# Performance work log

Hardware: AMD Instinct MI355X
Metric: run time of the kernel (lower is better)

## Reference

```python
import jax, jax.numpy as jnp
import numpy as np

DIM_INPUT = 1024
DIM_LATENT = 1024
DIM_HEAD = 64
INNER = max(DIM_INPUT, DIM_LATENT)  # 1024
HEADS = INNER // DIM_HEAD           # 16
SCALE = DIM_HEAD ** -0.5
RMS_EPS = 1e-8
LN_EPS = 1e-5


def layernorm(x, w, b):
    mu = jnp.mean(x, axis=-1, keepdims=True)
    var = jnp.var(x, axis=-1, keepdims=True)
    return (x - mu) * jax.lax.rsqrt(var + LN_EPS) * w + b


def rmsnorm(x, gamma):
    # x / clamp(||x||_2 * d^-0.5, eps) * gamma  (per-head, last dim = DIM_HEAD)
    norm = jnp.linalg.norm(x, axis=-1, keepdims=True) * (DIM_HEAD ** -0.5)
    return x / jnp.maximum(norm, RMS_EPS) * gamma


def setup_inputs() -> dict:
    key = jax.random.key(0)
    ks = jax.random.split(key, 10)
    b, n, m = 4, 2048, 256
    x = jax.random.normal(ks[0], (b, n, DIM_INPUT), dtype=jnp.float32)
    latents_c1 = jax.random.normal(ks[1], (b, m, DIM_LATENT), dtype=jnp.float32)
    latents_c0 = jax.random.normal(ks[2], (b, m, DIM_LATENT), dtype=jnp.float32)
    consciousness_mask = jax.random.randint(ks[3], (b, n), 0, 2).astype(bool)
    s = 0.02
    Wq = jax.random.normal(ks[4], (DIM_LATENT, INNER), dtype=jnp.float32) * s
    Wkv = jax.random.normal(ks[5], (DIM_INPUT, 2 * INNER), dtype=jnp.float32) * s
    Wout = jax.random.normal(ks[6], (INNER, DIM_LATENT), dtype=jnp.float32) * s
    bout = jnp.zeros((DIM_LATENT,), dtype=jnp.float32)
    ln_x_w = jnp.ones((DIM_INPUT,), dtype=jnp.float32)
    ln_x_b = jnp.zeros((DIM_INPUT,), dtype=jnp.float32)
    ln_l_w = jnp.ones((DIM_LATENT,), dtype=jnp.float32)
    ln_l_b = jnp.zeros((DIM_LATENT,), dtype=jnp.float32)
    gamma_q = jnp.ones((DIM_HEAD,), dtype=jnp.float32)
    gamma_k = jnp.ones((DIM_HEAD,), dtype=jnp.float32)
    return dict(x=x, latents_c1=latents_c1, latents_c0=latents_c0,
                consciousness_mask=consciousness_mask,
                ln_x_w=ln_x_w, ln_x_b=ln_x_b, ln_l_w=ln_l_w, ln_l_b=ln_l_b,
                gamma_q=gamma_q, gamma_k=gamma_k,
                Wq=Wq, Wkv=Wkv, Wout=Wout, bout=bout)


def reference(x, latents_c1, latents_c0, consciousness_mask,
              ln_x_w, ln_x_b, ln_l_w, ln_l_b, gamma_q, gamma_k,
              Wq, Wkv, Wout, bout):
    b, n, _ = x.shape
    m = latents_c1.shape[1]
    x = layernorm(x, ln_x_w, ln_x_b)
    l1 = layernorm(latents_c1, ln_l_w, ln_l_b)
    l0 = layernorm(latents_c0, ln_l_w, ln_l_b)

    # projections -> heads
    q1 = (l1 @ Wq).reshape(b, m, HEADS, DIM_HEAD).transpose(0, 2, 1, 3)  # b h m d
    q0 = (l0 @ Wq).reshape(b, m, HEADS, DIM_HEAD).transpose(0, 2, 1, 3)
    kv = x @ Wkv                                                         # b n 2*inner
    k, v = jnp.split(kv, 2, axis=-1)
    k = k.reshape(b, n, HEADS, DIM_HEAD).transpose(0, 2, 1, 3)           # b h n d
    v = v.reshape(b, n, HEADS, DIM_HEAD).transpose(0, 2, 1, 3)

    qn1 = rmsnorm(q1, gamma_q) * SCALE
    qn0 = rmsnorm(q0, gamma_q) * SCALE
    kn = rmsnorm(k, gamma_k)

    attn1 = jnp.einsum('bhid,bhjd->bhij', qn1, kn)
    attn0 = jnp.einsum('bhid,bhjd->bhij', qn0, kn)

    neg = -jnp.finfo(attn1.dtype).max
    attn1 = jnp.where(consciousness_mask[:, None, None, :], attn1, neg)
    # NOTE: source only masks the c1 stream; c0 is left unmasked (faithful).

    attn1 = jax.nn.softmax(attn1, axis=-1)
    attn0 = jax.nn.softmax(attn0, axis=-1)

    o1 = jnp.einsum('bhij,bhjd->bhid', attn1, v).transpose(0, 2, 1, 3).reshape(b, m, INNER)
    o0 = jnp.einsum('bhij,bhjd->bhid', attn0, v).transpose(0, 2, 1, 3).reshape(b, m, INNER)
    return (o1 @ Wout + bout, o0 @ Wout + bout)
```

## Files before the change

### kernel.cpp

```cpp
#include <hip/hip_runtime.h>
#include <hip/hip_bf16.h>
#include <float.h>
#include <math.h>

#define BB 4
#define NN 2048
#define MM 256
#define DIN 1024
#define INNER 1024
#define NHEADS 16
#define DHEAD 64

typedef __attribute__((ext_vector_type(8))) short bf16x8;
typedef __attribute__((ext_vector_type(4))) float f32x4;
typedef __attribute__((ext_vector_type(4))) unsigned int u32x4;

__device__ __forceinline__ unsigned short f2bf(float f) {
    unsigned int u = __builtin_bit_cast(unsigned int, f);
    u = (u + 0x7fffu + ((u >> 16) & 1u)) >> 16;
    return (unsigned short)u;
}

__device__ __forceinline__ float fexp2(float x) {
#if __has_builtin(__builtin_amdgcn_exp2f)
    return __builtin_amdgcn_exp2f(x);
#else
    float r; asm("v_exp_f32 %0, %1" : "=v"(r) : "v"(x)); return r;
#endif
}

__device__ __forceinline__ unsigned int cvt_pk_bf16(float a, float b) {
    unsigned int r;
    asm("v_cvt_pk_bf16_f32 %0, %1, %2" : "=v"(r) : "v"(a), "v"(b));
    return r;
}

__device__ __forceinline__ void gload_lds16(const void* g, void* l) {
    __builtin_amdgcn_global_load_lds((__attribute__((address_space(1))) void*)(g),
                                     (__attribute__((address_space(3))) void*)(l),
                                     16, 0, 0);
}

#define LOG2E 1.4426950408889634f

__global__ __launch_bounds__(256) void ln_all_kernel(const float* __restrict__ x,
                                                     const float* __restrict__ lc1,
                                                     const float* __restrict__ lc0,
                                                     unsigned short* __restrict__ xnb,
                                                     unsigned short* __restrict__ latb,
                                                     const float* __restrict__ xw,
                                                     const float* __restrict__ xb,
                                                     const float* __restrict__ lw,
                                                     const float* __restrict__ lb) {
    const int row = blockIdx.x;
    const float* srow;
    unsigned short* drow;
    const float *w, *bv;
    if (row < BB * NN) {
        srow = x + (size_t)row * 1024; drow = xnb + (size_t)row * 1024;
        w = xw; bv = xb;
    } else {
        const int r2 = row - BB * NN;
        srow = (r2 < BB * MM) ? (lc1 + (size_t)r2 * 1024)
                              : (lc0 + (size_t)(r2 - BB * MM) * 1024);
        drow = latb + (size_t)r2 * 1024;
        w = lw; bv = lb;
    }
    const int tid = threadIdx.x;
    const float4 v = ((const float4*)srow)[tid];
    float sum = v.x + v.y + v.z + v.w;
    float sq  = v.x * v.x + v.y * v.y + v.z * v.z + v.w * v.w;
    #pragma unroll
    for (int off = 32; off; off >>= 1) {
        sum += __shfl_down(sum, off);
        sq  += __shfl_down(sq, off);
    }
    __shared__ float ls[4], lq[4];
    const int wv = tid >> 6;
    if ((tid & 63) == 0) { ls[wv] = sum; lq[wv] = sq; }
    __syncthreads();
    sum = ls[0] + ls[1] + ls[2] + ls[3];
    sq  = lq[0] + lq[1] + lq[2] + lq[3];
    const float mu  = sum * (1.0f / 1024.0f);
    const float var = sq * (1.0f / 1024.0f) - mu * mu;
    const float rs  = rsqrtf(var + 1e-5f);
    const float4 w4 = ((const float4*)w)[tid];
    const float4 b4 = ((const float4*)bv)[tid];
    ushort4 o;
    o.x = f2bf((v.x - mu) * rs * w4.x + b4.x);
    o.y = f2bf((v.y - mu) * rs * w4.y + b4.y);
    o.z = f2bf((v.z - mu) * rs * w4.z + b4.z);
    o.w = f2bf((v.w - mu) * rs * w4.w + b4.w);
    ((ushort4*)drow)[tid] = o;
}

__global__ __launch_bounds__(256) void transpose_all_kernel(const float* __restrict__ Wkv,
                                                            const float* __restrict__ Wq,
                                                            const float* __restrict__ Wout,
                                                            unsigned short* __restrict__ WkvT,
                                                            unsigned short* __restrict__ WqT,
                                                            unsigned short* __restrict__ WoutT) {
    const int z = blockIdx.z;
    const float* W;
    unsigned short* WT;
    int N;
    if (z == 0)      { W = Wkv;  WT = WkvT;  N = 2048; }
    else if (z == 1) { W = Wq;   WT = WqT;   N = 1024; }
    else             { W = Wout; WT = WoutT; N = 1024; }
    if (blockIdx.x * 32 >= N) return;
    const int K = 1024;
    __shared__ float t[32][33];
    const int k0 = blockIdx.y * 32, n0 = blockIdx.x * 32;
    const int tx = threadIdx.x & 31, ty8 = threadIdx.x >> 5;
    #pragma unroll
    for (int i = 0; i < 4; i++) {
        const int k = ty8 + i * 8;
        t[k][tx] = W[(size_t)(k0 + k) * N + n0 + tx];
    }
    __syncthreads();
    #pragma unroll
    for (int i = 0; i < 4; i++) {
        const int n = ty8 + i * 8;
        WT[(size_t)(n0 + n) * K + k0 + tx] = f2bf(t[tx][n]);
    }
}

__global__ __launch_bounds__(256) void v_transpose_bf16(const unsigned short* __restrict__ vbh,
                                                        unsigned short* __restrict__ vth) {
    __shared__ unsigned short t[32][34];
    const int n0 = blockIdx.x * 32;
    const int d0 = blockIdx.y * 32;
    const int bh = blockIdx.z;
    const int b = bh >> 4, h = bh & 15;
    const int tx = threadIdx.x & 31, ty8 = threadIdx.x >> 5;
    #pragma unroll
    for (int i = 0; i < 4; i++) {
        const int nr = ty8 + i * 8;
        t[nr][tx] = vbh[(size_t)(b * NN + n0 + nr) * 1024 + h * 64 + d0 + tx];
    }
    __syncthreads();
    #pragma unroll
    for (int i = 0; i < 4; i++) {
        const int dr = ty8 + i * 8;
        vth[((size_t)(b * 16 + h) * 64 + d0 + dr) * 2048 + n0 + tx] = t[tx][dr];
    }
}

#define GEMM_STAGE(buf, ktile)                                                        \
    {                                                                                 \
        unsigned short* Ab = &As[buf][0];                                             \
        unsigned short* Bb = &Bs[buf][0];                                             \
        _Pragma("unroll")                                                             \
        for (int e = 0; e < EA; e++) {                                                \
            const int r0 = (w * EA + e) * 16;                                         \
            gload_lds16(Ag + (size_t)(r0 + srow) * K + (ktile) * 32 + selt, &Ab[r0 * 32]); \
        }                                                                             \
        _Pragma("unroll")                                                             \
        for (int e = 0; e < 2; e++) {                                                 \
            const int r0 = (w * 2 + e) * 16;                                          \
            gload_lds16(Bg + (size_t)(r0 + srow) * K + (ktile) * 32 + selt, &Bb[r0 * 32]); \
        }                                                                             \
    }

#define GEMM_COMPUTE(buf)                                                             \
    {                                                                                 \
        const unsigned short* Ab = &As[buf][0];                                       \
        const unsigned short* Bb = &Bs[buf][0];                                       \
        bf16x8 af[MREP], bfv[4];                                                      \
        _Pragma("unroll")                                                             \
        for (int m = 0; m < MREP; m++)                                                \
            af[m] = *(const bf16x8*)&Ab[(wr * (BM / 2) + m * 16 + (l & 15)) * 32 + (l >> 4) * 8]; \
        _Pragma("unroll")                                                             \
        for (int n = 0; n < 4; n++)                                                   \
            bfv[n] = *(const bf16x8*)&Bb[(wc * 64 + n * 16 + (l & 15)) * 32 + (l >> 4) * 8]; \
        _Pragma("unroll")                                                             \
        for (int m = 0; m < MREP; m++)                                                \
            _Pragma("unroll")                                                         \
            for (int n = 0; n < 4; n++)                                               \
                acc[m][n] = __builtin_amdgcn_mfma_f32_16x16x32_bf16(af[m], bfv[n], acc[m][n], 0, 0, 0); \
    }

#define VM_LPS                                                                        \
    { if constexpr (BM == 128) asm volatile("s_waitcnt vmcnt(4)" ::: "memory");       \
      else                     asm volatile("s_waitcnt vmcnt(3)" ::: "memory"); }
#define VM_ZERO  asm volatile("s_waitcnt vmcnt(0)" ::: "memory");
#define BARRIER  __builtin_amdgcn_s_barrier();

template<int MODE, int BM>
__global__ __launch_bounds__(256) void gemm_bf16_kernel(const unsigned short* __restrict__ A,
                                                        const unsigned short* __restrict__ BT,
                                                        float* __restrict__ C,
                                                        unsigned short* __restrict__ outK,
                                                        unsigned short* __restrict__ outV,
                                                        int M, int N, int K,
                                                        const float* __restrict__ aux) {
    constexpr int MREP = BM / 32;
    constexpr int EA = BM / 64;
    __shared__ __align__(16) unsigned short As[3][BM * 32];
    __shared__ __align__(16) unsigned short Bs[3][128 * 32];
    const int tid = threadIdx.x;
    const int l = tid & 63, w = tid >> 6;
    const int wr = w >> 1, wc = w & 1;

    const int gx = gridDim.x;
    const int flat = blockIdx.y * gx + blockIdx.x;
    const int cpx = (gx * gridDim.y) >> 3;
    const int swz = (flat & 7) * cpx + (flat >> 3);
    const int rb = (swz / gx) * BM, cb = (swz % gx) * 128;

    f32x4 acc[MREP][4];
    #pragma unroll
    for (int m = 0; m < MREP; m++)
        #pragma unroll
        for (int n = 0; n < 4; n++) acc[m][n] = (f32x4){0.0f, 0.0f, 0.0f, 0.0f};

    const int srow = l >> 2;
    const int selt = (l & 3) * 8;
    const unsigned short* Ag = A + (size_t)rb * K;
    const unsigned short* Bg = BT + (size_t)cb * K;

    const int nt = K >> 5;
    GEMM_STAGE(0, 0);
    GEMM_STAGE(1, 1);
    VM_LPS;
    BARRIER;
    for (int i = 0; i < nt; i++) {
        const int bi = i - (i / 3) * 3;
        if (i + 2 < nt) {
            const int bs = (i + 2) - ((i + 2) / 3) * 3;
            GEMM_STAGE(bs, i + 2);
            GEMM_COMPUTE(bi);
            VM_LPS;
        } else {
            GEMM_COMPUTE(bi);
            VM_ZERO;
        }
        BARRIER;
    }

    const int lx = l & 15;
    const int col0 = cb + wc * 64;
    const int row0 = rb + wr * (BM / 2) + (l >> 4) * 4;

    if constexpr (MODE == 0) {
        #pragma unroll
        for (int m = 0; m < MREP; m++) {
            #pragma unroll
            for (int n = 0; n < 4; n++) {
                const int col = col0 + n * 16 + lx;
                const float badd = aux[col];
                #pragma unroll
                for (int r = 0; r < 4; r++)
                    C[(size_t)(row0 + m * 16 + r) * N + col] = acc[m][n][r] + badd;
            }
        }
    } else {
        const bool isK = (MODE == 2) || (col0 < (N >> 1));
        if (isK) {
            float g4[4];
            #pragma unroll
            for (int n = 0; n < 4; n++) g4[n] = aux[n * 16 + lx];
            const float fin = (MODE == 2) ? (0.125f * LOG2E) : 1.0f;
            #pragma unroll
            for (int m = 0; m < MREP; m++) {
                #pragma unroll
                for (int r = 0; r < 4; r++) {
                    float ss = 0.0f;
                    #pragma unroll
                    for (int n = 0; n < 4; n++) ss += acc[m][n][r] * acc[m][n][r];
                    ss += __shfl_xor(ss, 1);
                    ss += __shfl_xor(ss, 2);
                    ss += __shfl_xor(ss, 4);
                    ss += __shfl_xor(ss, 8);
                    const float inv = fin / fmaxf(sqrtf(ss) * 0.125f, 1e-8f);
                    const size_t rbase = (size_t)(row0 + m * 16 + r) * 1024 + col0;
                    #pragma unroll
                    for (int n = 0; n < 4; n++)
                        outK[rbase + n * 16 + lx] = f2bf(acc[m][n][r] * inv * g4[n]);
                }
            }
        } else {
            const int colv = col0 - 1024;
            #pragma unroll
            for (int m = 0; m < MREP; m++) {
                #pragma unroll
                for (int r = 0; r < 4; r++) {
                    const size_t rbase = (size_t)(row0 + m * 16 + r) * 1024 + colv;
                    #pragma unroll
                    for (int n = 0; n < 4; n++)
                        outV[rbase + n * 16 + lx] = f2bf(acc[m][n][r]);
                }
            }
        }
    }
}

__global__ __launch_bounds__(256) void attn_mfma_kernel(const unsigned short* __restrict__ qbh,
                                                        const unsigned short* __restrict__ kbh,
                                                        const unsigned short* __restrict__ vth,
                                                        const int* __restrict__ mask,
                                                        unsigned short* __restrict__ obuf) {
    const int bh = blockIdx.x;
    const int qt = blockIdx.y;
    const int sid = blockIdx.z;
    const int b = bh >> 4, h = bh & 15;
    const int tid = threadIdx.x;
    const int l = tid & 63, w = tid >> 6;
    const int lq = l & 15, g = l >> 4;

    __shared__ __align__(16) unsigned short KVs[2][8192];
    __shared__ int Ms[2][64];

    bf16x8 aq[2];
    const size_t qrow = (size_t)((sid * BB + b) * MM + qt * 64 + w * 16 + lq);
    #pragma unroll
    for (int ks = 0; ks < 2; ks++)
        aq[ks] = *(const bf16x8*)&qbh[qrow * 1024 + h * 64 + ks * 32 + g * 8];

    const int srow0 = tid >> 3, srow1 = (tid >> 3) + 32, sc8 = tid & 7;
    const unsigned short* kgb = kbh + (size_t)(b * NN) * 1024 + h * 64;
    const unsigned short* vgb = vth + ((size_t)(b * 16 + h) * 64) * 2048;
    bf16x8 kreg0, kreg1, vreg0, vreg1;
    int mreg = 0;

#define ATT_LOAD(t0)                                                                  \
    {                                                                                 \
        kreg0 = *(const bf16x8*)&kgb[(size_t)((t0) + srow0) * 1024 + sc8 * 8];        \
        kreg1 = *(const bf16x8*)&kgb[(size_t)((t0) + srow1) * 1024 + sc8 * 8];        \
        vreg0 = *(const bf16x8*)&vgb[(size_t)srow0 * 2048 + (t0) + sc8 * 8];          \
        vreg1 = *(const bf16x8*)&vgb[(size_t)srow1 * 2048 + (t0) + sc8 * 8];          \
        if (tid < 64) mreg = mask[b * NN + (t0) + tid];                               \
    }

#define ATT_WRITE(buf)                                                                \
    {                                                                                 \
        unsigned short* kd = &KVs[buf][0];                                            \
        *(bf16x8*)&kd[srow0 * 64 + ((sc8 ^ (srow0 & 7)) * 8)] = kreg0;                \
        *(bf16x8*)&kd[srow1 * 64 + ((sc8 ^ (srow1 & 7)) * 8)] = kreg1;                \
        unsigned short* vd = &KVs[buf][4096];                                         \
        *(bf16x8*)&vd[srow0 * 64 + ((sc8 ^ (srow0 & 7)) * 8)] = vreg0;                \
        *(bf16x8*)&vd[srow1 * 64 + ((sc8 ^ (srow1 & 7)) * 8)] = vreg1;                \
        if (tid < 64) Ms[buf][tid] = mreg;                                            \
    }

    f32x4 oacc[4];
    #pragma unroll
    for (int n = 0; n < 4; n++) oacc[n] = (f32x4){0.0f, 0.0f, 0.0f, 0.0f};
    float mrun = -FLT_MAX, lrun = 0.0f;

    ATT_LOAD(0);
    ATT_WRITE(0);
    __syncthreads();
    int cur = 0;

    for (int t0 = 0; t0 < NN; t0 += 64) {
        const bool nxt = (t0 + 64 < NN);
        if (nxt) ATT_LOAD(t0 + 64);

        const unsigned short* kcur = &KVs[cur][0];
        const unsigned short* vcur = &KVs[cur][4096];

        f32x4 st[4];
        #pragma unroll
        for (int j = 0; j < 4; j++) st[j] = (f32x4){0.0f, 0.0f, 0.0f, 0.0f};
        #pragma unroll
        for (int j = 0; j < 4; j++) {
            #pragma unroll
            for (int ks = 0; ks < 2; ks++) {
                const int row = j * 16 + lq;
                const bf16x8 kf = *(const bf16x8*)&kcur[row * 64 + (((ks * 4 + g) ^ (row & 7)) * 8)];
                st[j] = __builtin_amdgcn_mfma_f32_16x16x32_bf16(kf, aq[ks], st[j], 0, 0, 0);
            }
        }

        float p[4][4];
        #pragma unroll
        for (int j = 0; j < 4; j++) {
            if (sid == 0) {
                const int4 mj = *(const int4*)&Ms[cur][j * 16 + g * 4];
                p[j][0] = mj.x ? st[j][0] : -3.0e38f;
                p[j][1] = mj.y ? st[j][1] : -3.0e38f;
                p[j][2] = mj.z ? st[j][2] : -3.0e38f;
                p[j][3] = mj.w ? st[j][3] : -3.0e38f;
            } else {
                #pragma unroll
                for (int r = 0; r < 4; r++) p[j][r] = st[j][r];
            }
        }

        float mloc = fmaxf(fmaxf(p[0][0], p[0][1]), fmaxf(p[0][2], p[0][3]));
        #pragma unroll
        for (int j = 1; j < 4; j++)
            mloc = fmaxf(mloc, fmaxf(fmaxf(p[j][0], p[j][1]), fmaxf(p[j][2], p[j][3])));
        mloc = fmaxf(mloc, __shfl_xor(mloc, 16));
        mloc = fmaxf(mloc, __shfl_xor(mloc, 32));

        if (__any(mloc > mrun + 8.0f)) {
            const float mn = fmaxf(mrun, mloc);
            const float scal = fexp2(mrun - mn);
            mrun = mn;
            lrun *= scal;
            float oscal[4];
            #pragma unroll
            for (int r = 0; r < 4; r++) oscal[r] = __shfl(scal, g * 4 + r);
            #pragma unroll
            for (int n = 0; n < 4; n++)
                #pragma unroll
                for (int r = 0; r < 4; r++) oacc[n][r] *= oscal[r];
        }

        float rsum = 0.0f;
        #pragma unroll
        for (int j = 0; j < 4; j++)
            #pragma unroll
            for (int r = 0; r < 4; r++) { p[j][r] = fexp2(p[j][r] - mrun); rsum += p[j][r]; }
        rsum += __shfl_xor(rsum, 16);
        rsum += __shfl_xor(rsum, 32);
        lrun += rsum;

        unsigned int packed[4][2];
        #pragma unroll
        for (int jt = 0; jt < 4; jt++)
            #pragma unroll
            for (int hh = 0; hh < 2; hh++)
                packed[jt][hh] = cvt_pk_bf16(p[jt][2 * hh], p[jt][2 * hh + 1]);

        #pragma unroll
        for (int ks = 0; ks < 2; ks++) {
            unsigned int wds[4];
            #pragma unroll
            for (int wd = 0; wd < 4; wd++) {
                const int src = lq + 16 * ((g & 1) * 2 + (wd >> 1));
                const unsigned int vA = (unsigned int)__shfl((int)packed[ks * 2][wd & 1], src);
                const unsigned int vB = (unsigned int)__shfl((int)packed[ks * 2 + 1][wd & 1], src);
                wds[wd] = (g & 2) ? vB : vA;
            }
            const u32x4 tmp = {wds[0], wds[1], wds[2], wds[3]};
            const bf16x8 afP = __builtin_bit_cast(bf16x8, tmp);
            #pragma unroll
            for (int n = 0; n < 4; n++) {
                const int drow = n * 16 + lq;
                const bf16x8 bv = *(const bf16x8*)&vcur[drow * 64 + (((ks * 4 + g) ^ (drow & 7)) * 8)];
                oacc[n] = __builtin_amdgcn_mfma_f32_16x16x32_bf16(afP, bv, oacc[n], 0, 0, 0);
            }
        }

        if (nxt) {
            ATT_WRITE(cur ^ 1);
            __syncthreads();
        }
        cur ^= 1;
    }

    const float il = 1.0f / lrun;
    float linv[4];
    #pragma unroll
    for (int r = 0; r < 4; r++) linv[r] = __shfl(il, g * 4 + r);
    unsigned short* ob = obuf + ((size_t)((sid * BB + b) * MM + qt * 64 + w * 16)) * 1024 + h * 64;
    #pragma unroll
    for (int n = 0; n < 4; n++)
        #pragma unroll
        for (int r = 0; r < 4; r++)
            ob[(size_t)(g * 4 + r) * 1024 + n * 16 + lq] = f2bf(oacc[n][r] * linv[r]);
}

extern "C" void kernel_launch(void* const* d_in, const int* in_sizes, int n_in,
                              void* d_out, int out_size, void* d_ws, size_t ws_size,
                              hipStream_t stream) {
    const float* x      = (const float*)d_in[0];
    const float* lc1    = (const float*)d_in[1];
    const float* lc0    = (const float*)d_in[2];
    const int*   mask   = (const int*)d_in[3];
    const float* ln_x_w = (const float*)d_in[4];
    const float* ln_x_b = (const float*)d_in[5];
    const float* ln_l_w = (const float*)d_in[6];
    const float* ln_l_b = (const float*)d_in[7];
    const float* g_q    = (const float*)d_in[8];
    const float* g_k    = (const float*)d_in[9];
    const float* Wq     = (const float*)d_in[10];
    const float* Wkv    = (const float*)d_in[11];
    const float* Wout   = (const float*)d_in[12];
    const float* bout   = (const float*)d_in[13];
    float* out = (float*)d_out;

    char* p = (char*)d_ws;
    unsigned short* xnb   = (unsigned short*)p; p += (size_t)8388608 * 2;
    unsigned short* latb  = (unsigned short*)p; p += (size_t)2097152 * 2;
    unsigned short* obb   = (unsigned short*)p; p += (size_t)2097152 * 2;
    unsigned short* WkvT  = (unsigned short*)p; p += (size_t)2097152 * 2;
    unsigned short* WqT   = (unsigned short*)p; p += (size_t)1048576 * 2;
    unsigned short* WoutT = (unsigned short*)p; p += (size_t)1048576 * 2;
    unsigned short* qbh   = (unsigned short*)p; p += (size_t)2097152 * 2;
    unsigned short* kbh   = (unsigned short*)p; p += (size_t)8388608 * 2;
    unsigned short* vbh   = (unsigned short*)p; p += (size_t)8388608 * 2;
    unsigned short* vth   = (unsigned short*)p; p += (size_t)8388608 * 2;

    ln_all_kernel<<<BB * NN + 2 * BB * MM, 256, 0, stream>>>(
        x, lc1, lc0, xnb, latb, ln_x_w, ln_x_b, ln_l_w, ln_l_b);

    transpose_all_kernel<<<dim3(64, 32, 3), 256, 0, stream>>>(
        Wkv, Wq, Wout, WkvT, WqT, WoutT);

    gemm_bf16_kernel<1, 128><<<dim3(2048 / 128, 8192 / 128), 256, 0, stream>>>(
        xnb, WkvT, nullptr, kbh, vbh, 8192, 2048, 1024, g_k);
    gemm_bf16_kernel<2, 64><<<dim3(1024 / 128, 2048 / 64), 256, 0, stream>>>(
        latb, WqT, nullptr, qbh, nullptr, 2048, 1024, 1024, g_q);

    v_transpose_bf16<<<dim3(NN / 32, 2, BB * NHEADS), 256, 0, stream>>>(vbh, vth);

    attn_mfma_kernel<<<dim3(BB * NHEADS, MM / 64, 2), 256, 0, stream>>>(qbh, kbh, vth, mask, obb);

    gemm_bf16_kernel<0, 64><<<dim3(1024 / 128, 2048 / 64), 256, 0, stream>>>(
        obb, WoutT, out, nullptr, nullptr, 2048, 1024, 1024, bout);
}
```

Before: 295.5 us.

## Share K/V tiles across both query streams and simplify GEMM to double buffering

The attention kernel now runs both query streams (c1 and c0) in one 512-thread block, so each K/V/mask tile is loaded into LDS once and used by 8 waves instead of being loaded separately by two blocks. This halves K/V global traffic for attention but halves the grid to 256 blocks and raises threads per block. The GEMM kernel's 3-stage pipeline with explicit vmcnt waits and raw barriers is replaced by a simpler 2-buffer ping-pong using __syncthreads, which likely waits for all loads each step and may reduce load/compute overlap.

```diff
diff --git a/kernel.cpp b/kernel.cpp
--- a/kernel.cpp
+++ b/kernel.cpp
@@ -146,45 +146,35 @@
     }
 }
 
-#define GEMM_STAGE(buf, ktile)                                                        \
+#define GEMM_STAGE(AS, BS, kt)                                                        \
     {                                                                                 \
-        unsigned short* Ab = &As[buf][0];                                             \
-        unsigned short* Bb = &Bs[buf][0];                                             \
         _Pragma("unroll")                                                             \
         for (int e = 0; e < EA; e++) {                                                \
             const int r0 = (w * EA + e) * 16;                                         \
-            gload_lds16(Ag + (size_t)(r0 + srow) * K + (ktile) * 32 + selt, &Ab[r0 * 32]); \
+            gload_lds16(Ag + (size_t)(r0 + srow) * K + (kt) + selt, &AS[r0 * 32]);    \
         }                                                                             \
         _Pragma("unroll")                                                             \
         for (int e = 0; e < 2; e++) {                                                 \
             const int r0 = (w * 2 + e) * 16;                                          \
-            gload_lds16(Bg + (size_t)(r0 + srow) * K + (ktile) * 32 + selt, &Bb[r0 * 32]); \
+            gload_lds16(Bg + (size_t)(r0 + srow) * K + (kt) + selt, &BS[r0 * 32]);    \
         }                                                                             \
     }
 
-#define GEMM_COMPUTE(buf)                                                             \
+#define GEMM_COMPUTE(AS, BS)                                                          \
     {                                                                                 \
-        const unsigned short* Ab = &As[buf][0];                                       \
-        const unsigned short* Bb = &Bs[buf][0];                                       \
         bf16x8 af[MREP], bfv[4];                                                      \
         _Pragma("unroll")                                                             \
         for (int m = 0; m < MREP; m++)                                                \
-            af[m] = *(const bf16x8*)&Ab[(wr * (BM / 2) + m * 16 + (l & 15)) * 32 + (l >> 4) * 8]; \
+            af[m] = *(const bf16x8*)&AS[(wr * (BM / 2) + m * 16 + (l & 15)) * 32 + (l >> 4) * 8]; \
         _Pragma("unroll")                                                             \
         for (int n = 0; n < 4; n++)                                                   \
-            bfv[n] = *(const bf16x8*)&Bb[(wc * 64 + n * 16 + (l & 15)) * 32 + (l >> 4) * 8]; \
+            bfv[n] = *(const bf16x8*)&BS[(wc * 64 + n * 16 + (l & 15)) * 32 + (l >> 4) * 8]; \
         _Pragma("unroll")                                                             \
         for (int m = 0; m < MREP; m++)                                                \
             _Pragma("unroll")                                                         \
             for (int n = 0; n < 4; n++)                                               \
                 acc[m][n] = __builtin_amdgcn_mfma_f32_16x16x32_bf16(af[m], bfv[n], acc[m][n], 0, 0, 0); \
     }
-
-#define VM_LPS                                                                        \
-    { if constexpr (BM == 128) asm volatile("s_waitcnt vmcnt(4)" ::: "memory");       \
-      else                     asm volatile("s_waitcnt vmcnt(3)" ::: "memory"); }
-#define VM_ZERO  asm volatile("s_waitcnt vmcnt(0)" ::: "memory");
-#define BARRIER  __builtin_amdgcn_s_barrier();
 
 template<int MODE, int BM>
 __global__ __launch_bounds__(256) void gemm_bf16_kernel(const unsigned short* __restrict__ A,
@@ -196,8 +186,10 @@
                                                         const float* __restrict__ aux) {
     constexpr int MREP = BM / 32;
     constexpr int EA = BM / 64;
-    __shared__ __align__(16) unsigned short As[3][BM * 32];
-    __shared__ __align__(16) unsigned short Bs[3][128 * 32];
+    __shared__ __align__(16) unsigned short As0[BM * 32];
+    __shared__ __align__(16) unsigned short As1[BM * 32];
+    __shared__ __align__(16) unsigned short Bs0[128 * 32];
+    __shared__ __align__(16) unsigned short Bs1[128 * 32];
     const int tid = threadIdx.x;
     const int l = tid & 63, w = tid >> 6;
     const int wr = w >> 1, wc = w & 1;
@@ -219,24 +211,21 @@
     const unsigned short* Ag = A + (size_t)rb * K;
     const unsigned short* Bg = BT + (size_t)cb * K;
 
-    const int nt = K >> 5;
-    GEMM_STAGE(0, 0);
-    GEMM_STAGE(1, 1);
-    VM_LPS;
-    BARRIER;
-    for (int i = 0; i < nt; i++) {
-        const int bi = i - (i / 3) * 3;
-        if (i + 2 < nt) {
-            const int bs = (i + 2) - ((i + 2) / 3) * 3;
-            GEMM_STAGE(bs, i + 2);
-            GEMM_COMPUTE(bi);
-            VM_LPS;
-        } else {
-            GEMM_COMPUTE(bi);
-            VM_ZERO;
-        }
-        BARRIER;
-    }
+    GEMM_STAGE(As0, Bs0, 0);
+    __syncthreads();
+    int kt = 0;
+    for (; kt + 64 < K; kt += 64) {
+        GEMM_STAGE(As1, Bs1, kt + 32);
+        GEMM_COMPUTE(As0, Bs0);
+        __syncthreads();
+        GEMM_STAGE(As0, Bs0, kt + 64);
+        GEMM_COMPUTE(As1, Bs1);
+        __syncthreads();
+    }
+    GEMM_STAGE(As1, Bs1, kt + 32);
+    GEMM_COMPUTE(As0, Bs0);
+    __syncthreads();
+    GEMM_COMPUTE(As1, Bs1);
 
     const int lx = l & 15;
     const int col0 = cb + wc * 64;
@@ -295,51 +284,46 @@
     }
 }
 
-__global__ __launch_bounds__(256) void attn_mfma_kernel(const unsigned short* __restrict__ qbh,
+__global__ __launch_bounds__(512) void attn_mfma_kernel(const unsigned short* __restrict__ qbh,
                                                         const unsigned short* __restrict__ kbh,
                                                         const unsigned short* __restrict__ vth,
                                                         const int* __restrict__ mask,
                                                         unsigned short* __restrict__ obuf) {
     const int bh = blockIdx.x;
     const int qt = blockIdx.y;
-    const int sid = blockIdx.z;
     const int b = bh >> 4, h = bh & 15;
     const int tid = threadIdx.x;
     const int l = tid & 63, w = tid >> 6;
+    const int sid = w >> 2;
+    const int wq = w & 3;
     const int lq = l & 15, g = l >> 4;
 
     __shared__ __align__(16) unsigned short KVs[2][8192];
     __shared__ int Ms[2][64];
 
     bf16x8 aq[2];
-    const size_t qrow = (size_t)((sid * BB + b) * MM + qt * 64 + w * 16 + lq);
+    const size_t qrow = (size_t)((sid * BB + b) * MM + qt * 64 + wq * 16 + lq);
     #pragma unroll
     for (int ks = 0; ks < 2; ks++)
         aq[ks] = *(const bf16x8*)&qbh[qrow * 1024 + h * 64 + ks * 32 + g * 8];
 
-    const int srow0 = tid >> 3, srow1 = (tid >> 3) + 32, sc8 = tid & 7;
+    const int srow = tid >> 3, sc8 = tid & 7;
     const unsigned short* kgb = kbh + (size_t)(b * NN) * 1024 + h * 64;
     const unsigned short* vgb = vth + ((size_t)(b * 16 + h) * 64) * 2048;
-    bf16x8 kreg0, kreg1, vreg0, vreg1;
+    bf16x8 kreg, vreg;
     int mreg = 0;
 
 #define ATT_LOAD(t0)                                                                  \
     {                                                                                 \
-        kreg0 = *(const bf16x8*)&kgb[(size_t)((t0) + srow0) * 1024 + sc8 * 8];        \
-        kreg1 = *(const bf16x8*)&kgb[(size_t)((t0) + srow1) * 1024 + sc8 * 8];        \
-        vreg0 = *(const bf16x8*)&vgb[(size_t)srow0 * 2048 + (t0) + sc8 * 8];          \
-        vreg1 = *(const bf16x8*)&vgb[(size_t)srow1 * 2048 + (t0) + sc8 * 8];          \
+        kreg = *(const bf16x8*)&kgb[(size_t)((t0) + srow) * 1024 + sc8 * 8];          \
+        vreg = *(const bf16x8*)&vgb[(size_t)srow * 2048 + (t0) + sc8 * 8];            \
         if (tid < 64) mreg = mask[b * NN + (t0) + tid];                               \
     }
 
 #define ATT_WRITE(buf)                                                                \
     {                                                                                 \
-        unsigned short* kd = &KVs[buf][0];                                            \
-        *(bf16x8*)&kd[srow0 * 64 + ((sc8 ^ (srow0 & 7)) * 8)] = kreg0;                \
-        *(bf16x8*)&kd[srow1 * 64 + ((sc8 ^ (srow1 & 7)) * 8)] = kreg1;                \
-        unsigned short* vd = &KVs[buf][4096];                                         \
-        *(bf16x8*)&vd[srow0 * 64 + ((sc8 ^ (srow0 & 7)) * 8)] = vreg0;                \
-        *(bf16x8*)&vd[srow1 * 64 + ((sc8 ^ (srow1 & 7)) * 8)] = vreg1;                \
+        *(bf16x8*)&KVs[buf][srow * 64 + ((sc8 ^ (srow & 7)) * 8)] = kreg;             \
+        *(bf16x8*)&KVs[buf][4096 + srow * 64 + ((sc8 ^ (srow & 7)) * 8)] = vreg;      \
         if (tid < 64) Ms[buf][tid] = mreg;                                            \
     }
 
@@ -456,7 +440,7 @@
     float linv[4];
     #pragma unroll
     for (int r = 0; r < 4; r++) linv[r] = __shfl(il, g * 4 + r);
-    unsigned short* ob = obuf + ((size_t)((sid * BB + b) * MM + qt * 64 + w * 16)) * 1024 + h * 64;
+    unsigned short* ob = obuf + ((size_t)((sid * BB + b) * MM + qt * 64 + wq * 16)) * 1024 + h * 64;
     #pragma unroll
     for (int n = 0; n < 4; n++)
         #pragma unroll
@@ -508,7 +492,7 @@
 
     v_transpose_bf16<<<dim3(NN / 32, 2, BB * NHEADS), 256, 0, stream>>>(vbh, vth);
 
-    attn_mfma_kernel<<<dim3(BB * NHEADS, MM / 64, 2), 256, 0, stream>>>(qbh, kbh, vth, mask, obb);
+    attn_mfma_kernel<<<dim3(BB * NHEADS, MM / 64), 512, 0, stream>>>(qbh, kbh, vth, mask, obb);
 
     gemm_bf16_kernel<0, 64><<<dim3(1024 / 128, 2048 / 64), 256, 0, stream>>>(
         obb, WoutT, out, nullptr, nullptr, 2048, 1024, 1024, bout);
```

Measured after the change: 247.1 us. 16.4% less time.
